# Optimization experiments

Hardware: AMD Instinct MI355X
Metric: run time of the kernel (lower is better)

Reference implementation:

```python
import jax, jax.numpy as jnp
from jax import lax
import numpy as np

# db4 (Daubechies-4) filters, matching pywt.Wavelet('db4')
L = 8
_REC_LO = np.array([0.23037781330885523, 0.7148465705525415, 0.6308807679295904,
                    -0.02798376941698385, -0.18703481171888114, 0.030841381835986965,
                    0.032883011666982945, -0.010597401784997278], dtype=np.float32)
_DEC_LO = _REC_LO[::-1].copy()
_DEC_HI = (((-1.0) ** (np.arange(L) + 1)) * _REC_LO).astype(np.float32)  # QMF
_REC_HI = _DEC_HI[::-1].copy()
# lax.conv performs correlation, so use reversed filters to get true convolution.
# rev(dec_lo)=rec_lo, rev(dec_hi)=rec_hi and vice versa.
DEC_K = jnp.asarray(np.stack([_DEC_LO[::-1], _DEC_HI[::-1]])[:, None, :])  # (2,1,L)
REC_K = jnp.asarray(np.stack([_REC_LO[::-1], _REC_HI[::-1]])[None, :, :])  # (1,2,L)

ENHANCE_FACTOR = 1.5
DENOISE_THRESHOLD = 0.2


def _dwt_last(x):
    # pywt single-level DWT (mode='symmetric') along last axis.
    # Equivalent to: conv(sym_pad(x, L-1), dec_filter)[valid][1::2]
    xe = jnp.pad(x, ((0, 0), (L - 1, L - 1)), mode='symmetric')[:, 1:]
    y = lax.conv_general_dilated(xe[:, None, :], DEC_K, (2,), 'VALID',
                                 dimension_numbers=('NCH', 'OIH', 'NCH'))
    return y[:, 0], y[:, 1]  # lo, hi, each (M, (S+L-1)//2)


def _idwt_last(lo, hi):
    # pywt single-level IDWT: upsample (lhs_dilation=2), filter, trim L-2 each side.
    c = jnp.stack([lo, hi], axis=1)  # (M, 2, n)
    y = lax.conv_general_dilated(c, REC_K, (1,), [(1, 1)], lhs_dilation=(2,),
                                 dimension_numbers=('NCH', 'OIH', 'NCH'))
    return y[:, 0]  # (M, 2n - L + 2)


def _dwt2(x):
    # x: (N, H, W) -> aa (cA), da (cH), ad (cV), dd (cD)
    N, H, W = x.shape
    lo, hi = _dwt_last(x.reshape(N * H, W))
    Wc = lo.shape[-1]
    lo = lo.reshape(N, H, Wc)
    hi = hi.reshape(N, H, Wc)

    def colwise(a):
        at = a.transpose(0, 2, 1).reshape(N * Wc, H)
        l, h = _dwt_last(at)
        Hc = l.shape[-1]
        return (l.reshape(N, Wc, Hc).transpose(0, 2, 1),
                h.reshape(N, Wc, Hc).transpose(0, 2, 1))

    aa, da = colwise(lo)
    ad, dd = colwise(hi)
    return aa, da, ad, dd


def _idwt2(aa, da, ad, dd):
    N, Hc, Wc = aa.shape

    def colinv(a, d):
        at = a.transpose(0, 2, 1).reshape(N * Wc, Hc)
        dt = d.transpose(0, 2, 1).reshape(N * Wc, Hc)
        r = _idwt_last(at, dt)
        H = r.shape[-1]
        return r.reshape(N, Wc, H).transpose(0, 2, 1)

    lo = colinv(aa, da)
    hi = colinv(ad, dd)
    H = lo.shape[1]
    out = _idwt_last(lo.reshape(N * H, Wc), hi.reshape(N * H, Wc))
    return out.reshape(N, H, -1)


def _soft_enhance(d):
    # enhance then pywt.threshold(..., mode='soft') with per-(image,channel,band) max
    d = d * ENHANCE_FACTOR
    t = DENOISE_THRESHOLD * jnp.max(jnp.abs(d), axis=(-2, -1), keepdims=True)
    return jnp.sign(d) * jnp.maximum(jnp.abs(d) - t, 0.0)


def setup_inputs() -> dict:
    key = jax.random.key(0)
    x = jax.random.normal(key, (32, 3, 510, 510), dtype=jnp.float32)
    return {'x': x}


def reference(x):
    B, C, H, W = x.shape
    z = x.reshape(B * C, H, W)
    a1, h1, v1, d1 = _dwt2(z)
    a2, h2, v2, d2 = _dwt2(a1)
    h2s, v2s, d2s = _soft_enhance(h2), _soft_enhance(v2), _soft_enhance(d2)
    h1s, v1s, d1s = _soft_enhance(h1), _soft_enhance(v1), _soft_enhance(d1)
    a1r = _idwt2(a2, h2s, v2s, d2s)
    out = _idwt2(a1r, h1s, v1s, d1s)
    return out.reshape(B, C, H, W)
```

## Files before the change

### kernel.cpp

```cpp
#include <hip/hip_runtime.h>

__device__ constexpr float DEC_LO[8] = {
    -0.010597401784997278f, 0.032883011666982945f, 0.030841381835986965f,
    -0.18703481171888114f, -0.02798376941698385f, 0.6308807679295904f,
    0.7148465705525415f, 0.23037781330885523f};
__device__ constexpr float DEC_HI[8] = {
    -0.23037781330885523f, 0.7148465705525415f, -0.6308807679295904f,
    -0.02798376941698385f, 0.18703481171888114f, 0.030841381835986965f,
    -0.032883011666982945f, -0.010597401784997278f};
__device__ constexpr float REC_LO[8] = {
    0.23037781330885523f, 0.7148465705525415f, 0.6308807679295904f,
    -0.02798376941698385f, -0.18703481171888114f, 0.030841381835986965f,
    0.032883011666982945f, -0.010597401784997278f};
__device__ constexpr float REC_HI[8] = {
    -0.010597401784997278f, -0.032883011666982945f, 0.030841381835986965f,
    0.18703481171888114f, -0.02798376941698385f, -0.6308807679295904f,
    0.7148465705525415f, -0.23037781330885523f};

__device__ __forceinline__ float soft_enh(float v, float th) {
    float e = 1.5f * v;
    float a = fabsf(e) - th;
    return a > 0.0f ? copysignf(a, e) : 0.0f;
}

#define TB 32
#define TO 64

#define RAWL_ROWS 70

__global__ __launch_bounds__(256, 4) void fused_dwt2_k(
    const float* __restrict__ x, int S, int Nc, int tiles,
    float* __restrict__ aa, float* __restrict__ da,
    float* __restrict__ ad, float* __restrict__ dd,
    unsigned* __restrict__ mx_da, unsigned* __restrict__ mx_ad,
    unsigned* __restrict__ mx_dd)
{
    int b = blockIdx.x;
    int tx = b % tiles, ty = (b / tiles) % tiles, m = b / (tiles * tiles);
    int jh0 = ty * TB, jw0 = tx * TB;
    int r0 = 2 * jh0 - 6, c0 = 2 * jw0 - 6;
    const float* xm = x + (size_t)m * S * S;

    __shared__ float rawL[RAWL_ROWS * 64];
    __shared__ float rawR[72 * 8];
    __shared__ float RB[70][68];

    int tid = threadIdx.x;
    int wv = tid >> 6, ln = tid & 63;

    auto refl = [S](int p) {
        p = p < 0 ? -1 - p : p;
        return p >= S ? 2 * S - 1 - p : p;
    };

    int pcL = refl(c0 + ln);
    for (int w = wv; w < RAWL_ROWS; w += 4) {
        int pr = refl(r0 + w);
        const float* g = xm + (size_t)pr * S + pcL;
#if defined(__has_builtin) && __has_builtin(__builtin_amdgcn_global_load_lds)
        __builtin_amdgcn_global_load_lds(
            (const __attribute__((address_space(1))) void*)g,
            (__attribute__((address_space(3))) void*)(&rawL[w << 6]),
            4, 0, 0);
#else
        rawL[(w << 6) + ln] = *g;
#endif
    }
    int pcR = refl(c0 + 64 + (ln & 7));
    int rsub = ln >> 3;
    for (int w = wv; w < 9; w += 4) {
        int r = (w << 3) + rsub;
        if (r > 69) r = 69;
        int pr = refl(r0 + r);
        const float* g = xm + (size_t)pr * S + pcR;
#if defined(__has_builtin) && __has_builtin(__builtin_amdgcn_global_load_lds)
        __builtin_amdgcn_global_load_lds(
            (const __attribute__((address_space(1))) void*)g,
            (__attribute__((address_space(3))) void*)(&rawR[w << 6]),
            4, 0, 0);
#else
        rawR[(w << 6) + ln] = *g;
#endif
    }
    __syncthreads();

    for (int e = tid; e < 560; e += 256) {
        int r = e >> 3, q = e & 7;
        float f[16];
        if (q < 7) {
            const float* base = &rawL[(r << 6) + (q << 3)];
            float4 A = *reinterpret_cast<const float4*>(base);
            float4 B = *reinterpret_cast<const float4*>(base + 4);
            float4 C = *reinterpret_cast<const float4*>(base + 8);
            float4 D = *reinterpret_cast<const float4*>(base + 12);
            f[0] = A.x; f[1] = A.y; f[2] = A.z; f[3] = A.w;
            f[4] = B.x; f[5] = B.y; f[6] = B.z; f[7] = B.w;
            f[8] = C.x; f[9] = C.y; f[10] = C.z; f[11] = C.w;
            f[12] = D.x; f[13] = D.y; f[14] = D.z; f[15] = D.w;
        } else {
            const float* bl = &rawL[(r << 6) + 56];
            float4 A = *reinterpret_cast<const float4*>(bl);
            float4 B = *reinterpret_cast<const float4*>(bl + 4);
            const float* br = &rawR[r << 3];
            float4 C = *reinterpret_cast<const float4*>(br);
            float2 D = *reinterpret_cast<const float2*>(br + 4);
            f[0] = A.x; f[1] = A.y; f[2] = A.z; f[3] = A.w;
            f[4] = B.x; f[5] = B.y; f[6] = B.z; f[7] = B.w;
            f[8] = C.x; f[9] = C.y; f[10] = C.z; f[11] = C.w;
            f[12] = D.x; f[13] = D.y; f[14] = 0.f; f[15] = 0.f;
        }
        float lo[4], hi[4];
#pragma unroll
        for (int i = 0; i < 4; ++i) {
            float alo = 0.f, ahi = 0.f;
#pragma unroll
            for (int t = 0; t < 8; ++t) {
                float v = f[2 * i + 7 - t];
                alo = fmaf(DEC_LO[t], v, alo);
                ahi = fmaf(DEC_HI[t], v, ahi);
            }
            lo[i] = alo; hi[i] = ahi;
        }
        int c4 = 4 * q;
        *reinterpret_cast<float4*>(&RB[r][c4]) = make_float4(lo[0], lo[1], lo[2], lo[3]);
        *reinterpret_cast<float4*>(&RB[r][32 + c4]) = make_float4(hi[0], hi[1], hi[2], hi[3]);
    }
    __syncthreads();

    int jj = tid & 31, g = tid >> 5;
    int jw = jw0 + jj;
    float mh = 0.f, mv = 0.f, md = 0.f;
#pragma unroll
    for (int pass = 0; pass < 2; ++pass) {
        int rbase = 8 * g + 4 * pass;
        float L[10], H[10];
#pragma unroll
        for (int rr = 0; rr < 10; ++rr) {
            L[rr] = RB[rbase + rr][jj];
            H[rr] = RB[rbase + rr][32 + jj];
        }
#pragma unroll
        for (int k = 0; k < 2; ++k) {
            float vaa = 0.f, vda = 0.f, vad = 0.f, vdd = 0.f;
#pragma unroll
            for (int t = 0; t < 8; ++t) {
                float l = L[2 * k + 7 - t];
                float h = H[2 * k + 7 - t];
                vaa = fmaf(DEC_LO[t], l, vaa);
                vda = fmaf(DEC_HI[t], l, vda);
                vad = fmaf(DEC_LO[t], h, vad);
                vdd = fmaf(DEC_HI[t], h, vdd);
            }
            int jh = jh0 + 4 * g + 2 * pass + k;
            if (jh < Nc && jw < Nc) {
                size_t o = ((size_t)m * Nc + jh) * Nc + jw;
                aa[o] = vaa; da[o] = vda; ad[o] = vad; dd[o] = vdd;
                mh = fmaxf(mh, fabsf(vda));
                mv = fmaxf(mv, fabsf(vad));
                md = fmaxf(md, fabsf(vdd));
            }
        }
    }
#pragma unroll
    for (int off = 32; off; off >>= 1) {
        mh = fmaxf(mh, __shfl_down(mh, off));
        mv = fmaxf(mv, __shfl_down(mv, off));
        md = fmaxf(md, __shfl_down(md, off));
    }
    __shared__ float sm[3][4];
    if (ln == 0) { sm[0][wv] = mh; sm[1][wv] = mv; sm[2][wv] = md; }
    __syncthreads();
    if (tid == 0) {
        float A = fmaxf(fmaxf(sm[0][0], sm[0][1]), fmaxf(sm[0][2], sm[0][3]));
        float B = fmaxf(fmaxf(sm[1][0], sm[1][1]), fmaxf(sm[1][2], sm[1][3]));
        float C = fmaxf(fmaxf(sm[2][0], sm[2][1]), fmaxf(sm[2][2], sm[2][3]));
        atomicMax(mx_da + m, __float_as_uint(A));
        atomicMax(mx_ad + m, __float_as_uint(B));
        atomicMax(mx_dd + m, __float_as_uint(C));
    }
}

__global__ __launch_bounds__(256, 4) void fused_idwt2_k(
    const float* __restrict__ a, const float* __restrict__ h,
    const float* __restrict__ v, const float* __restrict__ d,
    const unsigned* __restrict__ mxh, const unsigned* __restrict__ mxv,
    const unsigned* __restrict__ mxd,
    int n, int Ho, int tiles, float* __restrict__ out)
{
    int b = blockIdx.x;
    int tx = b % tiles, ty = (b / tiles) % tiles, m = b / (tiles * tiles);
    int i0 = ty * TO, u0 = tx * TO;
    int jr0 = i0 >> 1, jc0 = u0 >> 1;

    __shared__ float LH[TO][71];

    int tid = threadIdx.x;
    float th_h = 0.2f * (1.5f * __uint_as_float(mxh[m]));
    float th_v = 0.2f * (1.5f * __uint_as_float(mxv[m]));
    float th_d = 0.2f * (1.5f * __uint_as_float(mxd[m]));
    const float* am = a + (size_t)m * n * n;
    const float* hm = h + (size_t)m * n * n;
    const float* vm = v + (size_t)m * n * n;
    const float* dm = d + (size_t)m * n * n;

    auto coltask = [&](int task) {
        int g = task / 35, jc = task % 35;
        int jcg = jc0 + jc; if (jcg > n - 1) jcg = n - 1;
        float Ar[7], Hr[7], Vr[7], Dr[7];
#pragma unroll
        for (int rr = 0; rr < 7; ++rr) {
            int jr = jr0 + 4 * g + rr; if (jr > n - 1) jr = n - 1;
            size_t o = (size_t)jr * n + jcg;
            Ar[rr] = am[o];
            Hr[rr] = hm[o];
            Vr[rr] = vm[o];
            Dr[rr] = dm[o];
        }
#pragma unroll
        for (int rr = 0; rr < 7; ++rr) {
            Hr[rr] = soft_enh(Hr[rr], th_h);
            Vr[rr] = soft_enh(Vr[rr], th_v);
            Dr[rr] = soft_enh(Dr[rr], th_d);
        }
#pragma unroll
        for (int pass = 0; pass < 2; ++pass) {
            int P = 2 * g + pass;
            float acc_lo[4], acc_hi[4];
#pragma unroll
            for (int k = 0; k < 4; ++k) { acc_lo[k] = 0.f; acc_hi[k] = 0.f; }
#pragma unroll
            for (int rl = 0; rl < 5; ++rl) {
                int rr = 2 * pass + rl;
                float av = Ar[rr], hv = Hr[rr], vv = Vr[rr], dv = Dr[rr];
#pragma unroll
                for (int t = 0; t < 8; ++t) {
                    int k = 2 * rl + t - 6;
                    if (k >= 0 && k < 4) {
                        acc_lo[k] = fmaf(REC_LO[t], av, fmaf(REC_HI[t], hv, acc_lo[k]));
                        acc_hi[k] = fmaf(REC_LO[t], vv, fmaf(REC_HI[t], dv, acc_hi[k]));
                    }
                }
            }
#pragma unroll
            for (int k = 0; k < 4; ++k) {
                LH[4 * P + k][jc] = acc_lo[k];
                LH[4 * P + k][35 + jc] = acc_hi[k];
            }
        }
    };
    coltask(tid);
    if (tid + 256 < 8 * 35) coltask(tid + 256);
    __syncthreads();

    for (int e = tid; e < TO * TO; e += 256) {
        int il = e >> 6, ul = e & 63;
        int t0 = ul & 1;
        float acc = 0.f;
#pragma unroll
        for (int s = 0; s < 4; ++s) {
            int t = t0 + 2 * s;
            int c = (ul + 6 - t) >> 1;
            acc = fmaf(REC_LO[t], LH[il][c], acc);
            acc = fmaf(REC_HI[t], LH[il][35 + c], acc);
        }
        int gi = i0 + il, gu = u0 + ul;
        if (gi < Ho && gu < Ho)
            out[((size_t)m * Ho + gi) * Ho + gu] = acc;
    }
}

extern "C" void kernel_launch(void* const* d_in, const int* in_sizes, int n_in,
                              void* d_out, int out_size, void* d_ws, size_t ws_size,
                              hipStream_t stream) {
    const float* x = (const float*)d_in[0];
    float* out = (float*)d_out;
    float* ws = (float*)d_ws;

    const int M = 96, S1 = 510, N1 = 258, N2 = 132;
    const long S_l1 = (long)M * N1 * N1;
    const long S_l2 = (long)M * N2 * N2;

    float* aa1 = ws;
    float* h1  = aa1 + S_l1;
    float* v1  = h1 + S_l1;
    float* d1  = v1 + S_l1;
    float* a1r = d1 + S_l1;
    float* a2  = a1r + S_l1;
    float* h2  = a2 + S_l2;
    float* v2  = h2 + S_l2;
    float* d2  = v2 + S_l2;
    unsigned* th = (unsigned*)(d2 + S_l2);

    long need = 5 * S_l1 + 4 * S_l2 + 576;
    if (ws_size < (size_t)need * sizeof(float)) return;

    unsigned *th_h1 = th, *th_v1 = th + 96, *th_d1 = th + 192;
    unsigned *th_h2 = th + 288, *th_v2 = th + 384, *th_d2 = th + 480;

    hipMemsetAsync(th, 0, 576 * sizeof(unsigned), stream);

    fused_dwt2_k<<<9 * 9 * M, 256, 0, stream>>>(x, S1, N1, 9, aa1, h1, v1, d1,
                                                th_h1, th_v1, th_d1);
    fused_dwt2_k<<<5 * 5 * M, 256, 0, stream>>>(aa1, N1, N2, 5, a2, h2, v2, d2,
                                                th_h2, th_v2, th_d2);
    fused_idwt2_k<<<5 * 5 * M, 256, 0, stream>>>(a2, h2, v2, d2, th_h2, th_v2, th_d2,
                                                 N2, N1, 5, a1r);
    fused_idwt2_k<<<8 * 8 * M, 256, 0, stream>>>(a1r, h1, v1, d1, th_h1, th_v1, th_d1,
                                                 N1, S1, 8, out);
}
```

Baseline: 342.3 us.

## Store wavelet subbands transposed and vectorize subband writes and reads along rows

The forward DWT kernel now writes its four subbands in transposed (column-major) order. It pairs two adjacent output rows into float2 stores. The inverse kernel reads its 7-row column window as contiguous float2 loads on interior tiles and keeps a clamped scalar fallback at the edges. This trades the previous coalesced row-wise access across threads for fewer, wider per-thread accesses, so adjacent lanes now hit addresses a full row stride apart. That risks poor memory coalescing.

```diff
diff --git a/kernel.cpp b/kernel.cpp
--- a/kernel.cpp
+++ b/kernel.cpp
@@ -25,7 +25,6 @@
 
 #define TB 32
 #define TO 64
-
 #define RAWL_ROWS 70
 
 __global__ __launch_bounds__(256, 4) void fused_dwt2_k(
@@ -139,6 +138,7 @@
             L[rr] = RB[rbase + rr][jj];
             H[rr] = RB[rbase + rr][32 + jj];
         }
+        float va[2], vh_[2], vv_[2], vd_[2];
 #pragma unroll
         for (int k = 0; k < 2; ++k) {
             float vaa = 0.f, vda = 0.f, vad = 0.f, vdd = 0.f;
@@ -151,13 +151,24 @@
                 vad = fmaf(DEC_LO[t], h, vad);
                 vdd = fmaf(DEC_HI[t], h, vdd);
             }
-            int jh = jh0 + 4 * g + 2 * pass + k;
-            if (jh < Nc && jw < Nc) {
-                size_t o = ((size_t)m * Nc + jh) * Nc + jw;
-                aa[o] = vaa; da[o] = vda; ad[o] = vad; dd[o] = vdd;
-                mh = fmaxf(mh, fabsf(vda));
-                mv = fmaxf(mv, fabsf(vad));
-                md = fmaxf(md, fabsf(vdd));
+            va[k] = vaa; vh_[k] = vda; vv_[k] = vad; vd_[k] = vdd;
+        }
+        int jh = jh0 + 4 * g + 2 * pass;
+        if (jw < Nc && jh < Nc) {
+            size_t o = ((size_t)m * Nc + jw) * Nc + jh;
+            if (jh + 1 < Nc) {
+                *reinterpret_cast<float2*>(aa + o) = make_float2(va[0], va[1]);
+                *reinterpret_cast<float2*>(da + o) = make_float2(vh_[0], vh_[1]);
+                *reinterpret_cast<float2*>(ad + o) = make_float2(vv_[0], vv_[1]);
+                *reinterpret_cast<float2*>(dd + o) = make_float2(vd_[0], vd_[1]);
+                mh = fmaxf(mh, fmaxf(fabsf(vh_[0]), fabsf(vh_[1])));
+                mv = fmaxf(mv, fmaxf(fabsf(vv_[0]), fabsf(vv_[1])));
+                md = fmaxf(md, fmaxf(fabsf(vd_[0]), fabsf(vd_[1])));
+            } else {
+                aa[o] = va[0]; da[o] = vh_[0]; ad[o] = vv_[0]; dd[o] = vd_[0];
+                mh = fmaxf(mh, fabsf(vh_[0]));
+                mv = fmaxf(mv, fabsf(vv_[0]));
+                md = fmaxf(md, fabsf(vd_[0]));
             }
         }
     }
@@ -203,18 +214,47 @@
     const float* vm = v + (size_t)m * n * n;
     const float* dm = d + (size_t)m * n * n;
 
+    bool interior = (jr0 + 34 <= n - 1);
+
     auto coltask = [&](int task) {
         int g = task / 35, jc = task % 35;
         int jcg = jc0 + jc; if (jcg > n - 1) jcg = n - 1;
+        int base = jr0 + 4 * g;
         float Ar[7], Hr[7], Vr[7], Dr[7];
-#pragma unroll
-        for (int rr = 0; rr < 7; ++rr) {
-            int jr = jr0 + 4 * g + rr; if (jr > n - 1) jr = n - 1;
-            size_t o = (size_t)jr * n + jcg;
-            Ar[rr] = am[o];
-            Hr[rr] = hm[o];
-            Vr[rr] = vm[o];
-            Dr[rr] = dm[o];
+        if (interior) {
+            size_t ob = (size_t)jcg * n + base;
+            const float* ap = am + ob;
+            const float* hp = hm + ob;
+            const float* vp = vm + ob;
+            const float* dp = dm + ob;
+            float2 t0, t1, t2;
+            t0 = *reinterpret_cast<const float2*>(ap);
+            t1 = *reinterpret_cast<const float2*>(ap + 2);
+            t2 = *reinterpret_cast<const float2*>(ap + 4);
+            Ar[0]=t0.x; Ar[1]=t0.y; Ar[2]=t1.x; Ar[3]=t1.y; Ar[4]=t2.x; Ar[5]=t2.y;
+            Ar[6] = ap[6];
+            t0 = *reinterpret_cast<const float2*>(hp);
+            t1 = *reinterpret_cast<const float2*>(hp + 2);
+            t2 = *reinterpret_cast<const float2*>(hp + 4);
+            Hr[0]=t0.x; Hr[1]=t0.y; Hr[2]=t1.x; Hr[3]=t1.y; Hr[4]=t2.x; Hr[5]=t2.y;
+            Hr[6] = hp[6];
+            t0 = *reinterpret_cast<const float2*>(vp);
+            t1 = *reinterpret_cast<const float2*>(vp + 2);
+            t2 = *reinterpret_cast<const float2*>(vp + 4);
+            Vr[0]=t0.x; Vr[1]=t0.y; Vr[2]=t1.x; Vr[3]=t1.y; Vr[4]=t2.x; Vr[5]=t2.y;
+            Vr[6] = vp[6];
+            t0 = *reinterpret_cast<const float2*>(dp);
+            t1 = *reinterpret_cast<const float2*>(dp + 2);
+            t2 = *reinterpret_cast<const float2*>(dp + 4);
+            Dr[0]=t0.x; Dr[1]=t0.y; Dr[2]=t1.x; Dr[3]=t1.y; Dr[4]=t2.x; Dr[5]=t2.y;
+            Dr[6] = dp[6];
+        } else {
+#pragma unroll
+            for (int rr = 0; rr < 7; ++rr) {
+                int jr = base + rr; if (jr > n - 1) jr = n - 1;
+                size_t o = (size_t)jcg * n + jr;
+                Ar[rr] = am[o]; Hr[rr] = hm[o]; Vr[rr] = vm[o]; Dr[rr] = dm[o];
+            }
         }
 #pragma unroll
         for (int rr = 0; rr < 7; ++rr) {
```

Measured after the change: 389.8 us. +13.9%, slower.
